# Kernel optimization log

Measured on AMD Instinct MI355X. Metric: run time of the kernel, lower is better.

The kernel has to match this reference:

```python
import jax, jax.numpy as jnp
import numpy as np

B, N, DIN, DOUT = 16, 256, 64, 64
TEMP = 2.0          # temperatures[0]
POOL_K = 0.5        # pool_ratios[0]
BN_EPS = 1e-5


def setup_inputs() -> dict:
    key = jax.random.key(0)
    ks = jax.random.split(key, 8)
    g = lambda i, shape: (jax.random.normal(ks[i], shape, jnp.float32) * 0.08)
    return {
        "x": jax.random.normal(ks[0], (B, N, DIN), jnp.float32),
        # GraphAttentionLayer params
        "W_att": g(1, (DIN, DOUT)), "b_att": jnp.zeros((DOUT,), jnp.float32),
        "att_w": g(2, (DOUT,)),                      # att_weight [DOUT,1] squeezed
        "W_pwa": g(3, (DIN, DOUT)), "b_pwa": jnp.zeros((DOUT,), jnp.float32),
        "W_pna": g(4, (DIN, DOUT)), "b_pna": jnp.zeros((DOUT,), jnp.float32),
        "bn_scale": jnp.ones((DOUT,), jnp.float32),
        "bn_bias": jnp.zeros((DOUT,), jnp.float32),
        # GraphPool params
        "pool_w": g(5, (DOUT,)), "pool_b": jnp.zeros((), jnp.float32),
    }


def reference(x, W_att, b_att, att_w, W_pwa, b_pwa, W_pna, b_pna,
              bn_scale, bn_bias, pool_w, pool_b):
    # --- GraphAttentionLayer (eval mode: dropout = identity) ---
    # pairwise node multiplication: [B, i, j, DIN]
    pm = x[:, :, None, :] * x[:, None, :, :]
    att = jnp.tanh(jnp.einsum('bijd,de->bije', pm, W_att) + b_att)   # [B,N,N,DOUT]
    logits = jnp.einsum('bije,e->bij', att, att_w) / TEMP            # [B,N,N]
    # torch softmax over dim=-2 of [B,i,j,1] == axis j (the aggregated axis)
    A = jax.nn.softmax(logits, axis=2)                               # [B,N,N]
    agg = jnp.einsum('bij,bjd->bid', A, x)                           # [B,N,DIN]
    h = (agg @ W_pwa + b_pwa) + (x @ W_pna + b_pna)                  # [B,N,DOUT]
    # BatchNorm1d eval with running_mean=0, running_var=1
    h = h * (bn_scale / jnp.sqrt(1.0 + BN_EPS)) + bn_bias
    h = jax.nn.selu(h)
    # --- GraphPool (eval mode: dropout = identity) ---
    scores = jax.nn.sigmoid(h @ pool_w + pool_b)                     # [B,N]
    k = max(int(N * POOL_K), 1)
    _, idx = jax.lax.top_k(scores, k)                                # [B,k]
    hw = h * scores[:, :, None]
    out = jnp.take_along_axis(hw, idx[:, :, None], axis=1)           # [B,k,DOUT]
    return out
```

## Files before the change

kernel.cpp:

```cpp
#include <hip/hip_runtime.h>
#include <hip/hip_bf16.h>
#include <math.h>

#define BB 16
#define NN 256
#define DD 64
#define KTOP 128

typedef short s16x8 __attribute__((ext_vector_type(8)));
typedef float f32x4 __attribute__((ext_vector_type(4)));

typedef union { s16x8 v; unsigned u[4]; } frag_u;
typedef union { __hip_bfloat162 b2; unsigned u; } cvu;

__device__ __forceinline__ float asf(unsigned u){ union{unsigned u;float f;}c; c.u=u; return c.f; }

__device__ __forceinline__ void split2(float v0, float v1, unsigned& hu, unsigned& lu) {
    cvu c; c.b2 = __float22bfloat162_rn(make_float2(v0, v1));
    unsigned h = c.u;
    float l0 = v0 - asf(h << 16);
    float l1 = v1 - asf(h & 0xffff0000u);
    c.b2 = __float22bfloat162_rn(make_float2(l0, l1));
    hu = h; lu = c.u;
}

__global__ __launch_bounds__(512, 6) void k_fused(
    const float* __restrict__ x, const float* __restrict__ W_att,
    const float* __restrict__ b_att, const float* __restrict__ att_w,
    const float* __restrict__ Wpwa, const float* __restrict__ bpwa,
    const float* __restrict__ Wpna, const float* __restrict__ bpna,
    const float* __restrict__ bnsc, const float* __restrict__ bnbi,
    const float* __restrict__ poolw, const float* __restrict__ poolb,
    float* __restrict__ hbuf, float* __restrict__ scores)
{
    const int ig = blockIdx.x;
    const int b  = blockIdx.y;
    const int tid = threadIdx.x;
    const int w = tid >> 6, lane = tid & 63;
    const int quad = lane >> 4, c16 = lane & 15;
    const int jb = w * 32;
    const int ibase = ig * 8;

    __shared__ s16x8 sB[2][2][4][2][64];
    __shared__ float sXi[8 * 64];
    __shared__ float sL[8][256];
    __shared__ float sAgg[8][64];
    __shared__ float sBatt[64];
    __shared__ float sAww[64];

    sXi[tid] = x[(b * NN + ibase + (tid >> 6)) * DD + (tid & 63)];
    if (tid < 64) sBatt[tid] = b_att[tid];
    else if (tid < 128) sAww[tid - 64] = att_w[tid - 64];

    const float L2E2 = 2.8853900817779268f;

    float halfS;
    {
        float sa = 0.0f;
        #pragma unroll
        for (int mt = 0; mt < 4; ++mt) {
            float4 a4 = ((const float4*)att_w)[mt * 4 + quad];
            sa += (a4.x + a4.y) + (a4.z + a4.w);
        }
        sa += __shfl_xor(sa, 16);
        sa += __shfl_xor(sa, 32);
        halfS = 0.5f * sa;
    }

    const int bks = w >> 2, bmt = w & 3;

    frag_u Xh[2][2], Xl[2][2];
    #pragma unroll
    for (int jt = 0; jt < 2; ++jt) {
        #pragma unroll
        for (int ks = 0; ks < 2; ++ks) {
            const float* xr = &x[(b * NN + jb + jt * 16 + c16) * DD + ks * 32 + quad * 8];
            float4 a0 = *(const float4*)xr;
            float4 a1 = *(const float4*)(xr + 4);
            split2(a0.x, a0.y, Xh[jt][ks].u[0], Xl[jt][ks].u[0]);
            split2(a0.z, a0.w, Xh[jt][ks].u[1], Xl[jt][ks].u[1]);
            split2(a1.x, a1.y, Xh[jt][ks].u[2], Xl[jt][ks].u[2]);
            split2(a1.z, a1.w, Xh[jt][ks].u[3], Xl[jt][ks].u[3]);
        }
    }
    __syncthreads();

    {
        const float* xr = &sXi[0 * 64 + bks * 32 + quad * 8];
        float4 c0 = *(const float4*)xr;
        float4 c1 = *(const float4*)(xr + 4);
        float xiv[8] = {c0.x,c0.y,c0.z,c0.w,c1.x,c1.y,c1.z,c1.w};
        const float* wp = &W_att[(bks * 32 + quad * 8) * 64 + bmt * 16 + c16];
        frag_u bh, bl;
        split2(wp[0] * xiv[0], wp[64] * xiv[1], bh.u[0], bl.u[0]);
        split2(wp[128] * xiv[2], wp[192] * xiv[3], bh.u[1], bl.u[1]);
        split2(wp[256] * xiv[4], wp[320] * xiv[5], bh.u[2], bl.u[2]);
        split2(wp[384] * xiv[6], wp[448] * xiv[7], bh.u[3], bl.u[3]);
        sB[0][bks][bmt][0][lane] = bh.v;
        sB[0][bks][bmt][1][lane] = bl.v;
    }

    for (int ii = 0; ii < 8; ++ii) {
        __syncthreads();

        if (ii < 7) {
            const float* xr = &sXi[(ii + 1) * 64 + bks * 32 + quad * 8];
            float4 c0 = *(const float4*)xr;
            float4 c1 = *(const float4*)(xr + 4);
            float xiv[8] = {c0.x,c0.y,c0.z,c0.w,c1.x,c1.y,c1.z,c1.w};
            const float* wp = &W_att[(bks * 32 + quad * 8) * 64 + bmt * 16 + c16];
            frag_u bh, bl;
            split2(wp[0] * xiv[0], wp[64] * xiv[1], bh.u[0], bl.u[0]);
            split2(wp[128] * xiv[2], wp[192] * xiv[3], bh.u[1], bl.u[1]);
            split2(wp[256] * xiv[4], wp[320] * xiv[5], bh.u[2], bl.u[2]);
            split2(wp[384] * xiv[6], wp[448] * xiv[7], bh.u[3], bl.u[3]);
            sB[(ii + 1) & 1][bks][bmt][0][lane] = bh.v;
            sB[(ii + 1) & 1][bks][bmt][1][lane] = bl.v;
        }

        const int cur = ii & 1;
        float s0 = 0.0f, s1 = 0.0f;

        #pragma unroll
        for (int eth = 0; eth < 2; ++eth) {
            f32x4 acc[2][2];
            #pragma unroll
            for (int e2 = 0; e2 < 2; ++e2) {
                f32x4 bi = *(const f32x4*)&sBatt[(eth * 2 + e2) * 16 + quad * 4];
                acc[e2][0] = bi;
                acc[e2][1] = bi;
            }
            #pragma unroll
            for (int ks = 0; ks < 2; ++ks) {
                #pragma unroll
                for (int e2 = 0; e2 < 2; ++e2) {
                    const int mt = eth * 2 + e2;
                    s16x8 ah = sB[cur][ks][mt][0][lane];
                    s16x8 al = sB[cur][ks][mt][1][lane];
                    #pragma unroll
                    for (int jt = 0; jt < 2; ++jt) {
                        acc[e2][jt] = __builtin_amdgcn_mfma_f32_16x16x32_bf16(ah, Xh[jt][ks].v, acc[e2][jt], 0, 0, 0);
                        acc[e2][jt] = __builtin_amdgcn_mfma_f32_16x16x32_bf16(al, Xh[jt][ks].v, acc[e2][jt], 0, 0, 0);
                        acc[e2][jt] = __builtin_amdgcn_mfma_f32_16x16x32_bf16(ah, Xl[jt][ks].v, acc[e2][jt], 0, 0, 0);
                    }
                }
            }
            #pragma unroll
            for (int e2 = 0; e2 < 2; ++e2) {
                const int mt = eth * 2 + e2;
                f32x4 awwv = *(const f32x4*)&sAww[mt * 16 + quad * 4];
                #pragma unroll
                for (int r = 0; r < 4; ++r) {
                    {
                        float m = __builtin_amdgcn_exp2f(acc[e2][0][r] * L2E2);
                        s0 = fmaf(awwv[r], __builtin_amdgcn_rcpf(m + 1.0f), s0);
                    }
                    {
                        float m = __builtin_amdgcn_exp2f(acc[e2][1][r] * L2E2);
                        s1 = fmaf(awwv[r], __builtin_amdgcn_rcpf(m + 1.0f), s1);
                    }
                }
            }
        }

        s0 += __shfl_xor(s0, 16);
        s0 += __shfl_xor(s0, 32);
        s1 += __shfl_xor(s1, 16);
        s1 += __shfl_xor(s1, 32);
        if (quad == 0) {
            sL[ii][jb + c16]      = halfS - s0;
            sL[ii][jb + 16 + c16] = halfS - s1;
        }
    }
    __syncthreads();

    {
        const int i = ibase + w;
        float* row = sL[w];
        float lg0 = row[lane], lg1 = row[lane + 64], lg2 = row[lane + 128], lg3 = row[lane + 192];
        float m = fmaxf(fmaxf(lg0, lg1), fmaxf(lg2, lg3));
        #pragma unroll
        for (int off = 32; off; off >>= 1) m = fmaxf(m, __shfl_xor(m, off));
        float e0 = __expf(lg0 - m), e1 = __expf(lg1 - m), e2 = __expf(lg2 - m), e3 = __expf(lg3 - m);
        float ssum = (e0 + e1) + (e2 + e3);
        #pragma unroll
        for (int off = 32; off; off >>= 1) ssum += __shfl_xor(ssum, off);
        float inv = 1.0f / ssum;
        row[lane] = e0 * inv; row[lane + 64] = e1 * inv;
        row[lane + 128] = e2 * inv; row[lane + 192] = e3 * inv;
        __asm__ volatile("s_waitcnt lgkmcnt(0)" ::: "memory");

        float ag0 = 0.f, ag1 = 0.f, ag2 = 0.f, ag3 = 0.f;
        const float4* A4 = (const float4*)row;
        const float* xb = &x[(b * NN) * DD];
        #pragma unroll 8
        for (int jq = 0; jq < 64; ++jq) {
            float4 a = A4[jq];
            int j = jq * 4;
            ag0 = fmaf(a.x, xb[(j + 0) * DD + lane], ag0);
            ag1 = fmaf(a.y, xb[(j + 1) * DD + lane], ag1);
            ag2 = fmaf(a.z, xb[(j + 2) * DD + lane], ag2);
            ag3 = fmaf(a.w, xb[(j + 3) * DD + lane], ag3);
        }
        sAgg[w][lane] = (ag0 + ag1) + (ag2 + ag3);
        __asm__ volatile("s_waitcnt lgkmcnt(0)" ::: "memory");

        double h0 = 0.0, h1 = 0.0, h2 = 0.0, h3 = 0.0;
        #pragma unroll 4
        for (int d = 0; d < 64; d += 4) {
            h0 += (double)sAgg[w][d + 0] * (double)Wpwa[(d + 0) * DD + lane]
                + (double)sXi[w * 64 + d + 0] * (double)Wpna[(d + 0) * DD + lane];
            h1 += (double)sAgg[w][d + 1] * (double)Wpwa[(d + 1) * DD + lane]
                + (double)sXi[w * 64 + d + 1] * (double)Wpna[(d + 1) * DD + lane];
            h2 += (double)sAgg[w][d + 2] * (double)Wpwa[(d + 2) * DD + lane]
                + (double)sXi[w * 64 + d + 2] * (double)Wpna[(d + 2) * DD + lane];
            h3 += (double)sAgg[w][d + 3] * (double)Wpwa[(d + 3) * DD + lane]
                + (double)sXi[w * 64 + d + 3] * (double)Wpna[(d + 3) * DD + lane];
        }
        double hacc = ((double)bpwa[lane] + (double)bpna[lane]) + ((h0 + h1) + (h2 + h3));
        const double bnmul = 0.99999500003749968750e0;
        double hb = hacc * ((double)bnsc[lane] * bnmul) + (double)bnbi[lane];
        float hf = (float)hb;
        const float LAM = 1.0507009873554805f, ALP = 1.6732632423543772f;
        float hs = hf > 0.0f ? LAM * hf : LAM * ALP * (__expf(hf) - 1.0f);
        hbuf[(b * NN + i) * DD + lane] = hs;

        double z = (double)hs * (double)poolw[lane];
        #pragma unroll
        for (int off = 32; off; off >>= 1) z += __shfl_xor(z, off);
        if (lane == 0) {
            double zz = z + (double)poolb[0];
            scores[b * NN + i] = (float)(1.0 / (1.0 + exp(-zz)));
        }
    }
}

__global__ __launch_bounds__(256) void k_topk(
    const float* __restrict__ scores, const float* __restrict__ hbuf,
    float* __restrict__ out)
{
    const int c = blockIdx.x;
    const int b = blockIdx.y;
    const int t = threadIdx.x;
    __shared__ float ss[256];
    __shared__ int   perm[16];
    ss[t] = scores[b * NN + t];
    __syncthreads();
    const float my = ss[t];
    int rank = 0;
    #pragma unroll 8
    for (int j = 0; j < 256; ++j) {
        float v = ss[j];
        rank += (v > my) || (v == my && j < t);
    }
    if ((rank >> 4) == c) perm[rank & 15] = t;
    __syncthreads();
    #pragma unroll
    for (int m = t; m < 16 * DD; m += 256) {
        int r = m >> 6, e = m & 63;
        int i = perm[r];
        out[(b * KTOP + c * 16 + r) * DD + e] = hbuf[(b * NN + i) * DD + e] * ss[i];
    }
}

extern "C" void kernel_launch(void* const* d_in, const int* in_sizes, int n_in,
                              void* d_out, int out_size, void* d_ws, size_t ws_size,
                              hipStream_t stream) {
    const float* x        = (const float*)d_in[0];
    const float* W_att    = (const float*)d_in[1];
    const float* b_att    = (const float*)d_in[2];
    const float* att_w    = (const float*)d_in[3];
    const float* W_pwa    = (const float*)d_in[4];
    const float* b_pwa    = (const float*)d_in[5];
    const float* W_pna    = (const float*)d_in[6];
    const float* b_pna    = (const float*)d_in[7];
    const float* bn_scale = (const float*)d_in[8];
    const float* bn_bias  = (const float*)d_in[9];
    const float* pool_w   = (const float*)d_in[10];
    const float* pool_b   = (const float*)d_in[11];

    float* hbuf    = (float*)d_ws;
    float* scoresW = hbuf + BB * NN * DD;
    float* out     = (float*)d_out;

    k_fused<<<dim3(32, BB), 512, 0, stream>>>(x, W_att, b_att, att_w,
                                              W_pwa, b_pwa, W_pna, b_pna,
                                              bn_scale, bn_bias, pool_w, pool_b,
                                              hbuf, scoresW);
    k_topk<<<dim3(8, BB), 256, 0, stream>>>(scoresW, hbuf, out);
}
```

Baseline: 141.7 us.

## Halve rows per block, prebuild all B fragments and drop per-row barriers

Each block now handles 4 query rows instead of 8, doubling the grid to 64x16 blocks. All four rows' split-bf16 W_att·x_i fragments are built up front into a 4-deep shared buffer behind a single barrier, replacing the double-buffered loop that synchronised on every row. W_att values are loaded into registers once. The accumulator tile widens to 4x2, and launch bounds drop to 4 blocks per SM to leave room for the extra registers. In exchange, each block reloads and splits the full x_j operand for half as many rows, and half the waves sit idle in the softmax/aggregation stage.

```diff
diff --git a/kernel.cpp b/kernel.cpp
--- a/kernel.cpp
+++ b/kernel.cpp
@@ -24,7 +24,7 @@
     hu = h; lu = c.u;
 }
 
-__global__ __launch_bounds__(512, 6) void k_fused(
+__global__ __launch_bounds__(512, 4) void k_fused(
     const float* __restrict__ x, const float* __restrict__ W_att,
     const float* __restrict__ b_att, const float* __restrict__ att_w,
     const float* __restrict__ Wpwa, const float* __restrict__ bpwa,
@@ -39,16 +39,16 @@
     const int w = tid >> 6, lane = tid & 63;
     const int quad = lane >> 4, c16 = lane & 15;
     const int jb = w * 32;
-    const int ibase = ig * 8;
-
-    __shared__ s16x8 sB[2][2][4][2][64];
-    __shared__ float sXi[8 * 64];
-    __shared__ float sL[8][256];
-    __shared__ float sAgg[8][64];
+    const int ibase = ig * 4;
+
+    __shared__ s16x8 sB[4][2][4][2][64];
+    __shared__ float sXi[4 * 64];
+    __shared__ float sL[4][256];
+    __shared__ float sAgg[4][64];
     __shared__ float sBatt[64];
     __shared__ float sAww[64];
 
-    sXi[tid] = x[(b * NN + ibase + (tid >> 6)) * DD + (tid & 63)];
+    if (tid < 256) sXi[tid] = x[(b * NN + ibase + (tid >> 6)) * DD + (tid & 63)];
     if (tid < 64) sBatt[tid] = b_att[tid];
     else if (tid < 128) sAww[tid - 64] = att_w[tid - 64];
 
@@ -68,6 +68,13 @@
     }
 
     const int bks = w >> 2, bmt = w & 3;
+
+    float wv[8];
+    {
+        const float* wp = &W_att[(bks * 32 + quad * 8) * 64 + bmt * 16 + c16];
+        #pragma unroll
+        for (int t = 0; t < 8; ++t) wv[t] = wp[t * 64];
+    }
 
     frag_u Xh[2][2], Xl[2][2];
     #pragma unroll
@@ -85,80 +92,59 @@
     }
     __syncthreads();
 
-    {
-        const float* xr = &sXi[0 * 64 + bks * 32 + quad * 8];
+    #pragma unroll
+    for (int ii = 0; ii < 4; ++ii) {
+        const float* xr = &sXi[ii * 64 + bks * 32 + quad * 8];
         float4 c0 = *(const float4*)xr;
         float4 c1 = *(const float4*)(xr + 4);
         float xiv[8] = {c0.x,c0.y,c0.z,c0.w,c1.x,c1.y,c1.z,c1.w};
-        const float* wp = &W_att[(bks * 32 + quad * 8) * 64 + bmt * 16 + c16];
         frag_u bh, bl;
-        split2(wp[0] * xiv[0], wp[64] * xiv[1], bh.u[0], bl.u[0]);
-        split2(wp[128] * xiv[2], wp[192] * xiv[3], bh.u[1], bl.u[1]);
-        split2(wp[256] * xiv[4], wp[320] * xiv[5], bh.u[2], bl.u[2]);
-        split2(wp[384] * xiv[6], wp[448] * xiv[7], bh.u[3], bl.u[3]);
-        sB[0][bks][bmt][0][lane] = bh.v;
-        sB[0][bks][bmt][1][lane] = bl.v;
-    }
-
-    for (int ii = 0; ii < 8; ++ii) {
-        __syncthreads();
-
-        if (ii < 7) {
-            const float* xr = &sXi[(ii + 1) * 64 + bks * 32 + quad * 8];
-            float4 c0 = *(const float4*)xr;
-            float4 c1 = *(const float4*)(xr + 4);
-            float xiv[8] = {c0.x,c0.y,c0.z,c0.w,c1.x,c1.y,c1.z,c1.w};
-            const float* wp = &W_att[(bks * 32 + quad * 8) * 64 + bmt * 16 + c16];
-            frag_u bh, bl;
-            split2(wp[0] * xiv[0], wp[64] * xiv[1], bh.u[0], bl.u[0]);
-            split2(wp[128] * xiv[2], wp[192] * xiv[3], bh.u[1], bl.u[1]);
-            split2(wp[256] * xiv[4], wp[320] * xiv[5], bh.u[2], bl.u[2]);
-            split2(wp[384] * xiv[6], wp[448] * xiv[7], bh.u[3], bl.u[3]);
-            sB[(ii + 1) & 1][bks][bmt][0][lane] = bh.v;
-            sB[(ii + 1) & 1][bks][bmt][1][lane] = bl.v;
-        }
-
-        const int cur = ii & 1;
-        float s0 = 0.0f, s1 = 0.0f;
-
-        #pragma unroll
-        for (int eth = 0; eth < 2; ++eth) {
-            f32x4 acc[2][2];
+        split2(wv[0] * xiv[0], wv[1] * xiv[1], bh.u[0], bl.u[0]);
+        split2(wv[2] * xiv[2], wv[3] * xiv[3], bh.u[1], bl.u[1]);
+        split2(wv[4] * xiv[4], wv[5] * xiv[5], bh.u[2], bl.u[2]);
+        split2(wv[6] * xiv[6], wv[7] * xiv[7], bh.u[3], bl.u[3]);
+        sB[ii][bks][bmt][0][lane] = bh.v;
+        sB[ii][bks][bmt][1][lane] = bl.v;
+    }
+    __syncthreads();
+
+    #pragma unroll
+    for (int ii = 0; ii < 4; ++ii) {
+        f32x4 acc[4][2];
+        #pragma unroll
+        for (int mt = 0; mt < 4; ++mt) {
+            f32x4 bi = *(const f32x4*)&sBatt[mt * 16 + quad * 4];
+            acc[mt][0] = bi;
+            acc[mt][1] = bi;
+        }
+        #pragma unroll
+        for (int ks = 0; ks < 2; ++ks) {
             #pragma unroll
-            for (int e2 = 0; e2 < 2; ++e2) {
-                f32x4 bi = *(const f32x4*)&sBatt[(eth * 2 + e2) * 16 + quad * 4];
-                acc[e2][0] = bi;
-                acc[e2][1] = bi;
-            }
-            #pragma unroll
-            for (int ks = 0; ks < 2; ++ks) {
+            for (int mt = 0; mt < 4; ++mt) {
+                s16x8 ah = sB[ii][ks][mt][0][lane];
+                s16x8 al = sB[ii][ks][mt][1][lane];
                 #pragma unroll
-                for (int e2 = 0; e2 < 2; ++e2) {
-                    const int mt = eth * 2 + e2;
-                    s16x8 ah = sB[cur][ks][mt][0][lane];
-                    s16x8 al = sB[cur][ks][mt][1][lane];
-                    #pragma unroll
-                    for (int jt = 0; jt < 2; ++jt) {
-                        acc[e2][jt] = __builtin_amdgcn_mfma_f32_16x16x32_bf16(ah, Xh[jt][ks].v, acc[e2][jt], 0, 0, 0);
-                        acc[e2][jt] = __builtin_amdgcn_mfma_f32_16x16x32_bf16(al, Xh[jt][ks].v, acc[e2][jt], 0, 0, 0);
-                        acc[e2][jt] = __builtin_amdgcn_mfma_f32_16x16x32_bf16(ah, Xl[jt][ks].v, acc[e2][jt], 0, 0, 0);
-                    }
+                for (int jt = 0; jt < 2; ++jt) {
+                    acc[mt][jt] = __builtin_amdgcn_mfma_f32_16x16x32_bf16(ah, Xh[jt][ks].v, acc[mt][jt], 0, 0, 0);
+                    acc[mt][jt] = __builtin_amdgcn_mfma_f32_16x16x32_bf16(al, Xh[jt][ks].v, acc[mt][jt], 0, 0, 0);
+                    acc[mt][jt] = __builtin_amdgcn_mfma_f32_16x16x32_bf16(ah, Xl[jt][ks].v, acc[mt][jt], 0, 0, 0);
                 }
             }
+        }
+
+        float s0 = 0.0f, s1 = 0.0f;
+        #pragma unroll
+        for (int mt = 0; mt < 4; ++mt) {
+            f32x4 awwv = *(const f32x4*)&sAww[mt * 16 + quad * 4];
             #pragma unroll
-            for (int e2 = 0; e2 < 2; ++e2) {
-                const int mt = eth * 2 + e2;
-                f32x4 awwv = *(const f32x4*)&sAww[mt * 16 + quad * 4];
-                #pragma unroll
-                for (int r = 0; r < 4; ++r) {
-                    {
-                        float m = __builtin_amdgcn_exp2f(acc[e2][0][r] * L2E2);
-                        s0 = fmaf(awwv[r], __builtin_amdgcn_rcpf(m + 1.0f), s0);
-                    }
-                    {
-                        float m = __builtin_amdgcn_exp2f(acc[e2][1][r] * L2E2);
-                        s1 = fmaf(awwv[r], __builtin_amdgcn_rcpf(m + 1.0f), s1);
-                    }
+            for (int r = 0; r < 4; ++r) {
+                {
+                    float m = __builtin_amdgcn_exp2f(acc[mt][0][r] * L2E2);
+                    s0 = fmaf(awwv[r], __builtin_amdgcn_rcpf(m + 1.0f), s0);
+                }
+                {
+                    float m = __builtin_amdgcn_exp2f(acc[mt][1][r] * L2E2);
+                    s1 = fmaf(awwv[r], __builtin_amdgcn_rcpf(m + 1.0f), s1);
                 }
             }
         }
@@ -174,7 +160,7 @@
     }
     __syncthreads();
 
-    {
+    if (w < 4) {
         const int i = ibase + w;
         float* row = sL[w];
         float lg0 = row[lane], lg1 = row[lane + 64], lg2 = row[lane + 128], lg3 = row[lane + 192];
@@ -283,7 +269,7 @@
     float* scoresW = hbuf + BB * NN * DD;
     float* out     = (float*)d_out;
 
-    k_fused<<<dim3(32, BB), 512, 0, stream>>>(x, W_att, b_att, att_w,
+    k_fused<<<dim3(64, BB), 512, 0, stream>>>(x, W_att, b_att, att_w,
                                               W_pwa, b_pwa, W_pna, b_pna,
                                               bn_scale, bn_bias, pool_w, pool_b,
                                               hbuf, scoresW);
```

Result: slower. 149.7 us (+5.6%).
